# Optimization experiments

Measured on AMD Instinct MI355X. Metric: run time of the kernel, lower is better.

Reference implementation:

```python
import jax, jax.numpy as jnp
import numpy as np
import math

B, N = 1, 512
C_S, C_Z, C_H, H, PQ, PV = 384, 128, 16, 12, 4, 8
INF, EPS = 100000.0, 1e-8


def setup_inputs() -> dict:
    key = jax.random.key(0)
    ks = jax.random.split(key, 16)
    sc = 0.02
    return {
        "s": jax.random.normal(ks[0], (B, N, C_S), jnp.float32),
        "z": jax.random.normal(ks[1], (B, N, N, C_Z), jnp.float32),
        "t_trans": jax.random.normal(ks[2], (B, N, 3), jnp.float32),
        "t_rots": jax.random.normal(ks[3], (B, N, 3, 3), jnp.float32),
        "mask": jnp.ones((B, N), jnp.float32),
        "Wq": jax.random.normal(ks[4], (C_S, H * C_H), jnp.float32) * sc,
        "bq": jnp.zeros((H * C_H,), jnp.float32),
        "Wkv": jax.random.normal(ks[5], (C_S, 2 * H * C_H), jnp.float32) * sc,
        "bkv": jnp.zeros((2 * H * C_H,), jnp.float32),
        "Wqp": jax.random.normal(ks[6], (C_S, H * PQ * 3), jnp.float32) * sc,
        "bqp": jnp.zeros((H * PQ * 3,), jnp.float32),
        "Wkvp": jax.random.normal(ks[7], (C_S, H * (PQ + PV) * 3), jnp.float32) * sc,
        "bkvp": jnp.zeros((H * (PQ + PV) * 3,), jnp.float32),
        "Wb": jax.random.normal(ks[8], (C_Z, H), jnp.float32) * sc,
        "bb": jnp.zeros((H,), jnp.float32),
        "head_weights": jnp.full((H,), 0.5413, jnp.float32),  # softplus^-1(1) init
        "Wout": jax.random.normal(ks[9], (H * (C_Z + C_H + PV * 4), C_S), jnp.float32) * sc,
        "bout": jnp.zeros((C_S,), jnp.float32),
    }


def _split3_stack(x):
    # torch.split into 3 chunks along -1, then stack on new last axis -> [..., P, 3]
    return jnp.stack(jnp.split(x, 3, axis=-1), axis=-1)


def reference(s, z, t_trans, t_rots, mask, Wq, bq, Wkv, bkv, Wqp, bqp, Wkvp, bkvp,
              Wb, bb, head_weights, Wout, bout):
    q = (s @ Wq + bq).reshape(B, N, H, C_H)
    kv = (s @ Wkv + bkv).reshape(B, N, H, 2 * C_H)
    k, v = kv[..., :C_H], kv[..., C_H:]

    # point projections, moved to global frame: r @ p + t
    qp = _split3_stack(s @ Wqp + bqp)                      # [B,N,H*PQ,3] local
    qp = jnp.einsum('bnij,bnpj->bnpi', t_rots, qp) + t_trans[:, :, None, :]
    q_pts = qp.reshape(B, N, H, PQ, 3)
    kvp = _split3_stack(s @ Wkvp + bkvp)                   # [B,N,H*(PQ+PV),3]
    kvp = jnp.einsum('bnij,bnpj->bnpi', t_rots, kvp) + t_trans[:, :, None, :]
    kvp = kvp.reshape(B, N, H, PQ + PV, 3)
    k_pts, v_pts = kvp[..., :PQ, :], kvp[..., PQ:, :]

    b = z @ Wb + bb                                        # [B,N,N,H]

    a = jnp.einsum('bihc,bjhc->bhij', q, k) * math.sqrt(1.0 / (3 * C_H))
    a = a + math.sqrt(1.0 / 3) * jnp.transpose(b, (0, 3, 1, 2))

    # point-distance attention: [B,N,N,H,PQ]
    d2 = jnp.sum((q_pts[:, :, None] - k_pts[:, None]) ** 2, axis=-1)
    hw = jax.nn.softplus(head_weights) * math.sqrt(1.0 / (3 * (PQ * 9.0 / 2)))
    a = a + (-0.5) * jnp.einsum('bijhp,h->bhij', d2, hw)

    square_mask = INF * (mask[:, :, None] * mask[:, None, :] - 1.0)  # [B,N,N]
    a = jax.nn.softmax(a + square_mask[:, None], axis=-1)  # [B,H,N,N]

    o = jnp.einsum('bhij,bjhc->bihc', a, v).reshape(B, N, H * C_H)

    o_pt = jnp.einsum('bhij,bjhpx->bihpx', a, v_pts)       # [B,N,H,PV,3] global
    # invert frame: r^T @ (p - t)
    o_pt = jnp.einsum('bnji,bnhpj->bnhpi', t_rots, o_pt - t_trans[:, :, None, None, :])
    o_pt_norm = jnp.sqrt(jnp.sum(o_pt ** 2, axis=-1) + EPS).reshape(B, N, H * PV)
    o_pt = o_pt.reshape(B, N, H * PV, 3)

    o_pair = jnp.einsum('bhij,bijc->bihc', a, z).reshape(B, N, H * C_Z)

    cat = jnp.concatenate(
        [o, o_pt[..., 0], o_pt[..., 1], o_pt[..., 2], o_pt_norm, o_pair], axis=-1)
    return cat @ Wout + bout
```

## Files before the change

### kernel.cpp

```cpp
#include <hip/hip_runtime.h>
#include <math.h>

#define N 512
#define CS 384
#define CZ 128
#define CH 16
#define NH 12
#define PQ 4
#define PV 8

#define OFF_Q     0
#define OFF_K     98304
#define OFF_V     196608
#define OFF_QRAW  294912
#define OFF_KVRAW 368640
#define OFF_QPTS  589824
#define OFF_KPTS  663552
#define OFF_VPTS  737280
#define OFF_A     884736
#define OFF_CAT   4030464

__global__ __launch_bounds__(128) void proj_kernel(
    const float* __restrict__ s,
    const float* __restrict__ Wq,  const float* __restrict__ bq,
    const float* __restrict__ Wkv, const float* __restrict__ bkv,
    const float* __restrict__ Wqp, const float* __restrict__ bqp,
    const float* __restrict__ Wkvp,const float* __restrict__ bkvp,
    float* __restrict__ ws)
{
    __shared__ float st[16 * CS];
    const int n0 = blockIdx.x * 16;
    for (int idx = threadIdx.x * 4; idx < 16 * CS; idx += 128 * 4)
        *(float4*)&st[idx] = *(const float4*)&s[n0 * CS + idx];
    __syncthreads();

    const int tc = threadIdx.x & 31;
    const int tr = threadIdx.x >> 5;
    const int u0 = blockIdx.y * 128 + tc * 4;
    const int r0 = tr * 4;

    const float* W; const float* bptr; int ncol, lc0;
    if (u0 < 192)      { W = Wq;   bptr = bq;   ncol = 192; lc0 = u0; }
    else if (u0 < 576) { W = Wkv;  bptr = bkv;  ncol = 384; lc0 = u0 - 192; }
    else if (u0 < 720) { W = Wqp;  bptr = bqp;  ncol = 144; lc0 = u0 - 576; }
    else               { W = Wkvp; bptr = bkvp; ncol = 432; lc0 = u0 - 720; }

    float acc[4][4];
    #pragma unroll
    for (int r = 0; r < 4; r++)
        #pragma unroll
        for (int c = 0; c < 4; c++) acc[r][c] = 0.f;

    for (int k = 0; k < CS; k += 4) {
        float4 w0 = *(const float4*)&W[(k + 0) * ncol + lc0];
        float4 w1 = *(const float4*)&W[(k + 1) * ncol + lc0];
        float4 w2 = *(const float4*)&W[(k + 2) * ncol + lc0];
        float4 w3 = *(const float4*)&W[(k + 3) * ncol + lc0];
        #pragma unroll
        for (int r = 0; r < 4; r++) {
            float4 sv = *(const float4*)&st[(r0 + r) * CS + k];
            acc[r][0] += sv.x * w0.x + sv.y * w1.x + sv.z * w2.x + sv.w * w3.x;
            acc[r][1] += sv.x * w0.y + sv.y * w1.y + sv.z * w2.y + sv.w * w3.y;
            acc[r][2] += sv.x * w0.z + sv.y * w1.z + sv.z * w2.z + sv.w * w3.z;
            acc[r][3] += sv.x * w0.w + sv.y * w1.w + sv.z * w2.w + sv.w * w3.w;
        }
    }

    #pragma unroll
    for (int c = 0; c < 4; c++) {
        const int u = u0 + c;
        const float bias = bptr[lc0 + c];
        #pragma unroll
        for (int r = 0; r < 4; r++) {
            const int n = n0 + r0 + r;
            int oidx;
            if (u < 192) oidx = OFF_Q + n * 192 + u;
            else if (u < 576) {
                int lc = u - 192, h = lc >> 5, w = lc & 31;
                oidx = (w < 16) ? OFF_K + n * 192 + h * 16 + w
                                : OFF_V + n * 192 + h * 16 + (w - 16);
            } else if (u < 720) oidx = OFF_QRAW + n * 144 + (u - 576);
            else                oidx = OFF_KVRAW + n * 432 + (u - 720);
            ws[oidx] = acc[r][c] + bias;
        }
    }
}

__global__ __launch_bounds__(192) void point_kernel(
    const float* __restrict__ t_trans, const float* __restrict__ t_rots,
    float* __restrict__ ws)
{
    const int n = blockIdx.x;
    const int t = threadIdx.x;
    __shared__ float R[9], tr[3];
    if (t < 9) R[t] = t_rots[n * 9 + t];
    if (t < 3) tr[t] = t_trans[n * 3 + t];
    __syncthreads();

    float x0, x1, x2;
    int base;
    if (t < 48) {
        int idx = t;
        x0 = ws[OFF_QRAW + n * 144 + 0 * 48 + idx];
        x1 = ws[OFF_QRAW + n * 144 + 1 * 48 + idx];
        x2 = ws[OFF_QRAW + n * 144 + 2 * 48 + idx];
        int h = idx >> 2, p = idx & 3;
        base = OFF_QPTS + ((n * NH + h) * PQ + p) * 3;
    } else {
        int idx = t - 48;
        x0 = ws[OFF_KVRAW + n * 432 + 0 * 144 + idx];
        x1 = ws[OFF_KVRAW + n * 432 + 1 * 144 + idx];
        x2 = ws[OFF_KVRAW + n * 432 + 2 * 144 + idx];
        int h = idx / 12, p = idx % 12;
        if (p < PQ) base = OFF_KPTS + ((n * NH + h) * PQ + p) * 3;
        else        base = OFF_VPTS + ((n * NH + h) * PV + (p - PQ)) * 3;
    }
    ws[base + 0] = R[0] * x0 + R[1] * x1 + R[2] * x2 + tr[0];
    ws[base + 1] = R[3] * x0 + R[4] * x1 + R[5] * x2 + tr[1];
    ws[base + 2] = R[6] * x0 + R[7] * x1 + R[8] * x2 + tr[2];
}

__global__ __launch_bounds__(192) void logitA_kernel(
    const float* __restrict__ mask, const float* __restrict__ hweights,
    float* __restrict__ ws)
{
    const int j0 = blockIdx.x * 16;
    const int i0 = blockIdx.y * 16;
    const int t = threadIdx.x;

    __shared__ float qt[16 * 200];
    __shared__ float kt[16 * 200];
    __shared__ float qpt[16 * 148];
    __shared__ float kpt[16 * 148];
    __shared__ float mi[16], mj[16];

    {
        const float* src = ws + OFF_Q + i0 * 192;
        for (int idx = t * 4; idx < 3072; idx += 768) {
            float4 v = *(const float4*)&src[idx];
            *(float4*)&qt[(idx / 192) * 200 + idx % 192] = v;
        }
    }
    {
        const float* src = ws + OFF_K + j0 * 192;
        for (int idx = t * 4; idx < 3072; idx += 768) {
            float4 v = *(const float4*)&src[idx];
            *(float4*)&kt[(idx / 192) * 200 + idx % 192] = v;
        }
    }
    {
        const float* src = ws + OFF_QPTS + i0 * 144;
        for (int idx = t * 4; idx < 2304; idx += 768) {
            float4 v = *(const float4*)&src[idx];
            *(float4*)&qpt[(idx / 144) * 148 + idx % 144] = v;
        }
    }
    {
        const float* src = ws + OFF_KPTS + j0 * 144;
        for (int idx = t * 4; idx < 2304; idx += 768) {
            float4 v = *(const float4*)&src[idx];
            *(float4*)&kpt[(idx / 144) * 148 + idx % 144] = v;
        }
    }
    if (t < 16) { mi[t] = mask[i0 + t]; mj[t] = mask[j0 + t]; }
    __syncthreads();

    const int jj = t & 15;
    const int h = t >> 4;
    const float hw = log1pf(expf(hweights[h])) * 0.13608276348795434f;
    const float cqk = 0.14433756729740643f;

    float4 kr0 = *(const float4*)&kt[jj * 200 + h * 16 + 0];
    float4 kr1 = *(const float4*)&kt[jj * 200 + h * 16 + 4];
    float4 kr2 = *(const float4*)&kt[jj * 200 + h * 16 + 8];
    float4 kr3 = *(const float4*)&kt[jj * 200 + h * 16 + 12];
    float4 kp0 = *(const float4*)&kpt[jj * 148 + h * 12 + 0];
    float4 kp1 = *(const float4*)&kpt[jj * 148 + h * 12 + 4];
    float4 kp2 = *(const float4*)&kpt[jj * 148 + h * 12 + 8];
    const float mjv = mj[jj];

    for (int ii = 0; ii < 16; ii++) {
        float4 q0 = *(const float4*)&qt[ii * 200 + h * 16 + 0];
        float4 q1 = *(const float4*)&qt[ii * 200 + h * 16 + 4];
        float4 q2 = *(const float4*)&qt[ii * 200 + h * 16 + 8];
        float4 q3 = *(const float4*)&qt[ii * 200 + h * 16 + 12];
        float qk = q0.x * kr0.x + q0.y * kr0.y + q0.z * kr0.z + q0.w * kr0.w
                 + q1.x * kr1.x + q1.y * kr1.y + q1.z * kr1.z + q1.w * kr1.w
                 + q2.x * kr2.x + q2.y * kr2.y + q2.z * kr2.z + q2.w * kr2.w
                 + q3.x * kr3.x + q3.y * kr3.y + q3.z * kr3.z + q3.w * kr3.w;
        float4 p0 = *(const float4*)&qpt[ii * 148 + h * 12 + 0];
        float4 p1 = *(const float4*)&qpt[ii * 148 + h * 12 + 4];
        float4 p2 = *(const float4*)&qpt[ii * 148 + h * 12 + 8];
        float e, d2 = 0.f;
        e = p0.x - kp0.x; d2 += e * e;  e = p0.y - kp0.y; d2 += e * e;
        e = p0.z - kp0.z; d2 += e * e;  e = p0.w - kp0.w; d2 += e * e;
        e = p1.x - kp1.x; d2 += e * e;  e = p1.y - kp1.y; d2 += e * e;
        e = p1.z - kp1.z; d2 += e * e;  e = p1.w - kp1.w; d2 += e * e;
        e = p2.x - kp2.x; d2 += e * e;  e = p2.y - kp2.y; d2 += e * e;
        e = p2.z - kp2.z; d2 += e * e;  e = p2.w - kp2.w; d2 += e * e;
        float sm = 100000.0f * (mi[ii] * mjv - 1.0f);
        ws[OFF_A + ((size_t)(i0 + ii) * NH + h) * N + j0 + jj] =
            qk * cqk - 0.5f * hw * d2 + sm;
    }
}

__global__ __launch_bounds__(512) void bsoft_kernel(
    const float* __restrict__ z, const float* __restrict__ Wb,
    const float* __restrict__ bb, float* __restrict__ ws)
{
    const int i = blockIdx.x;
    const int t = threadIdx.x;
    __shared__ float zt[128 * 132];
    __shared__ float wbt[12 * 132];
    __shared__ float wred[8][4];

    for (int idx = t; idx < CZ * NH; idx += 512) {
        int c = idx / NH, h = idx % NH;
        wbt[h * 132 + c] = Wb[idx];
    }

    const int jj = t & 127;
    const int hg = t >> 7;
    const int h0 = hg * 3;
    const float bb0 = bb[h0], bb1 = bb[h0 + 1], bb2 = bb[h0 + 2];
    const float cb = 0.5773502691896258f;

    float lg[3][4];

    for (int T = 0; T < 4; T++) {
        __syncthreads();
        const float* zsrc = z + ((size_t)i * N + T * 128) * CZ;
        for (int idx = t * 4; idx < 16384; idx += 2048) {
            float4 v = *(const float4*)&zsrc[idx];
            *(float4*)&zt[(idx >> 7) * 132 + (idx & 127)] = v;
        }
        __syncthreads();

        float a0 = bb0, a1 = bb1, a2 = bb2;
        const float* zr = &zt[jj * 132];
        const float* w0 = &wbt[(h0 + 0) * 132];
        const float* w1 = &wbt[(h0 + 1) * 132];
        const float* w2 = &wbt[(h0 + 2) * 132];
        #pragma unroll
        for (int c = 0; c < CZ; c += 4) {
            float4 zq = *(const float4*)&zr[c];
            float4 q0 = *(const float4*)&w0[c];
            float4 q1 = *(const float4*)&w1[c];
            float4 q2 = *(const float4*)&w2[c];
            a0 += zq.x * q0.x + zq.y * q0.y + zq.z * q0.z + zq.w * q0.w;
            a1 += zq.x * q1.x + zq.y * q1.y + zq.z * q1.z + zq.w * q1.w;
            a2 += zq.x * q2.x + zq.y * q2.y + zq.z * q2.z + zq.w * q2.w;
        }
        const float* arow = ws + OFF_A + (size_t)i * NH * N + T * 128 + jj;
        lg[0][T] = arow[(size_t)(h0 + 0) * N] + cb * a0;
        lg[1][T] = arow[(size_t)(h0 + 1) * N] + cb * a1;
        lg[2][T] = arow[(size_t)(h0 + 2) * N] + cb * a2;
    }

    const int wv = t >> 6;
    float mx[3], sm[3];
    #pragma unroll
    for (int r = 0; r < 3; r++) {
        float m = fmaxf(fmaxf(lg[r][0], lg[r][1]), fmaxf(lg[r][2], lg[r][3]));
        #pragma unroll
        for (int o = 32; o > 0; o >>= 1) m = fmaxf(m, __shfl_xor(m, o));
        mx[r] = m;
    }
    if ((t & 63) == 0) {
        wred[wv][0] = mx[0]; wred[wv][1] = mx[1]; wred[wv][2] = mx[2];
    }
    __syncthreads();
    #pragma unroll
    for (int r = 0; r < 3; r++)
        mx[r] = fmaxf(wred[hg * 2][r], wred[hg * 2 + 1][r]);
    __syncthreads();
    #pragma unroll
    for (int r = 0; r < 3; r++) {
        float s = 0.f;
        #pragma unroll
        for (int T = 0; T < 4; T++) { lg[r][T] = __expf(lg[r][T] - mx[r]); s += lg[r][T]; }
        #pragma unroll
        for (int o = 32; o > 0; o >>= 1) s += __shfl_xor(s, o);
        sm[r] = s;
    }
    if ((t & 63) == 0) {
        wred[wv][0] = sm[0]; wred[wv][1] = sm[1]; wred[wv][2] = sm[2];
    }
    __syncthreads();
    #pragma unroll
    for (int r = 0; r < 3; r++) {
        float inv = 1.0f / (wred[hg * 2][r] + wred[hg * 2 + 1][r]);
        float* prow = ws + OFF_A + ((size_t)i * NH + h0 + r) * N + jj;
        #pragma unroll
        for (int T = 0; T < 4; T++)
            prow[T * 128] = lg[r][T] * inv;
    }
}

__global__ __launch_bounds__(832) void finish_kernel(
    const float* __restrict__ z, const float* __restrict__ t_trans,
    const float* __restrict__ t_rots, const float* __restrict__ ws_c,
    float* __restrict__ ws)
{
    const int i = blockIdx.x;
    const int t = threadIdx.x;
    __shared__ float a_s[12 * 520];

    {
        const float* src = ws_c + OFF_A + (size_t)i * (NH * N);
        for (int idx = t * 4; idx < NH * N; idx += 832 * 4) {
            float4 v = *(const float4*)&src[idx];
            int h = idx >> 9, j = idx & 511;
            *(float4*)&a_s[h * 520 + j] = v;
        }
    }
    __syncthreads();

    float* cat = ws + OFF_CAT + (size_t)i * 2112;

    if (t < 512) {
        const int c = t & 127, hg = t >> 7;
        const float* zrow = z + (size_t)i * N * CZ + c;
        const float* a0 = a_s + (hg + 0) * 520;
        const float* a1 = a_s + (hg + 4) * 520;
        const float* a2 = a_s + (hg + 8) * 520;
        float acc0 = 0.f, acc1 = 0.f, acc2 = 0.f;
        #pragma unroll 8
        for (int j = 0; j < N; j++) {
            float zv = zrow[(size_t)j * CZ];
            acc0 += a0[j] * zv; acc1 += a1[j] * zv; acc2 += a2[j] * zv;
        }
        cat[576 + (hg + 0) * CZ + c] = acc0;
        cat[576 + (hg + 4) * CZ + c] = acc1;
        cat[576 + (hg + 8) * CZ + c] = acc2;
    } else if (t < 704) {
        const int u = t - 512, h = u >> 4, cc = u & 15;
        const float* vcol = ws_c + OFF_V + h * 16 + cc;
        const float* ah = a_s + h * 520;
        float acc = 0.f;
        #pragma unroll 8
        for (int j = 0; j < N; j++)
            acc += ah[j] * vcol[j * 192];
        cat[h * 16 + cc] = acc;
    } else if (t < 800) {
        const int u = t - 704, h = u >> 3, p = u & 7;
        const float* vp = ws_c + OFF_VPTS + (h * PV + p) * 3;
        const float* ah = a_s + h * 520;
        float g0 = 0.f, g1 = 0.f, g2 = 0.f;
        #pragma unroll 4
        for (int j = 0; j < N; j++) {
            float av = ah[j];
            const float* vpj = vp + j * (NH * PV * 3);
            g0 += av * vpj[0]; g1 += av * vpj[1]; g2 += av * vpj[2];
        }
        float R[9], ti[3];
        #pragma unroll
        for (int x = 0; x < 9; x++) R[x] = t_rots[i * 9 + x];
        #pragma unroll
        for (int x = 0; x < 3; x++) ti[x] = t_trans[i * 3 + x];
        g0 -= ti[0]; g1 -= ti[1]; g2 -= ti[2];
        float l0 = R[0] * g0 + R[3] * g1 + R[6] * g2;
        float l1 = R[1] * g0 + R[4] * g1 + R[7] * g2;
        float l2 = R[2] * g0 + R[5] * g1 + R[8] * g2;
        float nrm = sqrtf(l0 * l0 + l1 * l1 + l2 * l2 + 1e-8f);
        int e = h * PV + p;
        cat[192 + e] = l0;
        cat[288 + e] = l1;
        cat[384 + e] = l2;
        cat[480 + e] = nrm;
    }
}

__global__ __launch_bounds__(384) void init_out_kernel(
    const float* __restrict__ bout, float* __restrict__ out)
{
    out[(size_t)blockIdx.x * 384 + threadIdx.x] = bout[threadIdx.x];
}

__global__ __launch_bounds__(384) void out_kernel(
    const float* __restrict__ Wout, const float* __restrict__ ws,
    float* __restrict__ out)
{
    const int rt = blockIdx.x;
    const int kc = blockIdx.y;
    const int t = threadIdx.x;
    __shared__ float ct[16 * 264];
    for (int idx = t * 4; idx < 16 * 264; idx += 384 * 4) {
        int rr = idx / 264, kk = idx % 264;
        *(float4*)&ct[idx] =
            *(const float4*)&ws[OFF_CAT + (size_t)(rt * 16 + rr) * 2112 + kc * 264 + kk];
    }
    __syncthreads();
    const int cq = t % 96, rg = t / 96;
    const int c0 = cq * 4;
    float acc[4][4] = {};
    const float* Wp = Wout + (size_t)kc * 264 * 384 + c0;
    for (int kk = 0; kk < 264; kk++) {
        float4 w = *(const float4*)&Wp[(size_t)kk * 384];
        #pragma unroll
        for (int r = 0; r < 4; r++) {
            float sv = ct[(rg * 4 + r) * 264 + kk];
            acc[r][0] += sv * w.x; acc[r][1] += sv * w.y;
            acc[r][2] += sv * w.z; acc[r][3] += sv * w.w;
        }
    }
    #pragma unroll
    for (int r = 0; r < 4; r++) {
        float* op = out + (size_t)(rt * 16 + rg * 4 + r) * 384 + c0;
        atomicAdd(&op[0], acc[r][0]);
        atomicAdd(&op[1], acc[r][1]);
        atomicAdd(&op[2], acc[r][2]);
        atomicAdd(&op[3], acc[r][3]);
    }
}

extern "C" void kernel_launch(void* const* d_in, const int* in_sizes, int n_in,
                              void* d_out, int out_size, void* d_ws, size_t ws_size,
                              hipStream_t stream) {
    const float* s       = (const float*)d_in[0];
    const float* z       = (const float*)d_in[1];
    const float* t_trans = (const float*)d_in[2];
    const float* t_rots  = (const float*)d_in[3];
    const float* mask    = (const float*)d_in[4];
    const float* Wq      = (const float*)d_in[5];
    const float* bq      = (const float*)d_in[6];
    const float* Wkv     = (const float*)d_in[7];
    const float* bkv     = (const float*)d_in[8];
    const float* Wqp     = (const float*)d_in[9];
    const float* bqp     = (const float*)d_in[10];
    const float* Wkvp    = (const float*)d_in[11];
    const float* bkvp    = (const float*)d_in[12];
    const float* Wb      = (const float*)d_in[13];
    const float* bb      = (const float*)d_in[14];
    const float* hweights= (const float*)d_in[15];
    const float* Wout    = (const float*)d_in[16];
    const float* bout    = (const float*)d_in[17];
    float* ws  = (float*)d_ws;
    float* out = (float*)d_out;

    init_out_kernel<<<512, 384, 0, stream>>>(bout, out);
    proj_kernel<<<dim3(32, 9), 128, 0, stream>>>(s, Wq, bq, Wkv, bkv, Wqp, bqp, Wkvp, bkvp, ws);
    point_kernel<<<512, 192, 0, stream>>>(t_trans, t_rots, ws);
    logitA_kernel<<<dim3(32, 32), 192, 0, stream>>>(mask, hweights, ws);
    bsoft_kernel<<<512, 512, 0, stream>>>(z, Wb, bb, ws);
    finish_kernel<<<512, 832, 0, stream>>>(z, t_trans, t_rots, ws, ws);
    out_kernel<<<dim3(32, 8), 384, 0, stream>>>(Wout, ws, out);
}
```

Measured before the change: 425.4 us.

## Transpose V and point layouts, restructure pair-attention reduction, split proj/out work finer

```diff
diff --git a/kernel.cpp b/kernel.cpp
--- a/kernel.cpp
+++ b/kernel.cpp
@@ -11,16 +11,32 @@
 
 #define OFF_Q     0
 #define OFF_K     98304
-#define OFF_V     196608
 #define OFF_QRAW  294912
 #define OFF_KVRAW 368640
 #define OFF_QPTS  589824
 #define OFF_KPTS  663552
-#define OFF_VPTS  737280
+#define OFF_VPX   737280
+#define OFF_VPY   786432
+#define OFF_VPZ   835584
 #define OFF_A     884736
 #define OFF_CAT   4030464
-
-__global__ __launch_bounds__(128) void proj_kernel(
+#define OFF_VT    5111808
+#define OFF_WBT   5210112
+
+__global__ __launch_bounds__(384) void init_out_kernel(
+    const float* __restrict__ bout, const float* __restrict__ Wb,
+    float* __restrict__ out, float* __restrict__ ws)
+{
+    out[(size_t)blockIdx.x * 384 + threadIdx.x] = bout[threadIdx.x];
+    if (blockIdx.x == 0) {
+        for (int idx = threadIdx.x; idx < NH * CZ; idx += 384) {
+            int h = idx >> 7, c = idx & 127;
+            ws[OFF_WBT + idx] = Wb[c * NH + h];
+        }
+    }
+}
+
+__global__ __launch_bounds__(256) void proj_kernel(
     const float* __restrict__ s,
     const float* __restrict__ Wq,  const float* __restrict__ bq,
     const float* __restrict__ Wkv, const float* __restrict__ bkv,
@@ -30,14 +46,14 @@
 {
     __shared__ float st[16 * CS];
     const int n0 = blockIdx.x * 16;
-    for (int idx = threadIdx.x * 4; idx < 16 * CS; idx += 128 * 4)
+    for (int idx = threadIdx.x * 4; idx < 16 * CS; idx += 1024)
         *(float4*)&st[idx] = *(const float4*)&s[n0 * CS + idx];
     __syncthreads();
 
     const int tc = threadIdx.x & 31;
     const int tr = threadIdx.x >> 5;
     const int u0 = blockIdx.y * 128 + tc * 4;
-    const int r0 = tr * 4;
+    const int r0 = tr * 2;
 
     const float* W; const float* bptr; int ncol, lc0;
     if (u0 < 192)      { W = Wq;   bptr = bq;   ncol = 192; lc0 = u0; }
@@ -45,9 +61,9 @@
     else if (u0 < 720) { W = Wqp;  bptr = bqp;  ncol = 144; lc0 = u0 - 576; }
     else               { W = Wkvp; bptr = bkvp; ncol = 432; lc0 = u0 - 720; }
 
-    float acc[4][4];
-    #pragma unroll
-    for (int r = 0; r < 4; r++)
+    float acc[2][4];
+    #pragma unroll
+    for (int r = 0; r < 2; r++)
         #pragma unroll
         for (int c = 0; c < 4; c++) acc[r][c] = 0.f;
 
@@ -57,7 +73,7 @@
         float4 w2 = *(const float4*)&W[(k + 2) * ncol + lc0];
         float4 w3 = *(const float4*)&W[(k + 3) * ncol + lc0];
         #pragma unroll
-        for (int r = 0; r < 4; r++) {
+        for (int r = 0; r < 2; r++) {
             float4 sv = *(const float4*)&st[(r0 + r) * CS + k];
             acc[r][0] += sv.x * w0.x + sv.y * w1.x + sv.z * w2.x + sv.w * w3.x;
             acc[r][1] += sv.x * w0.y + sv.y * w1.y + sv.z * w2.y + sv.w * w3.y;
@@ -71,14 +87,14 @@
         const int u = u0 + c;
         const float bias = bptr[lc0 + c];
         #pragma unroll
-        for (int r = 0; r < 4; r++) {
+        for (int r = 0; r < 2; r++) {
             const int n = n0 + r0 + r;
             int oidx;
             if (u < 192) oidx = OFF_Q + n * 192 + u;
             else if (u < 576) {
                 int lc = u - 192, h = lc >> 5, w = lc & 31;
                 oidx = (w < 16) ? OFF_K + n * 192 + h * 16 + w
-                                : OFF_V + n * 192 + h * 16 + (w - 16);
+                                : OFF_VT + (h * 16 + (w - 16)) * 512 + n;
             } else if (u < 720) oidx = OFF_QRAW + n * 144 + (u - 576);
             else                oidx = OFF_KVRAW + n * 432 + (u - 720);
             ws[oidx] = acc[r][c] + bias;
@@ -98,26 +114,35 @@
     __syncthreads();
 
     float x0, x1, x2;
-    int base;
     if (t < 48) {
         int idx = t;
         x0 = ws[OFF_QRAW + n * 144 + 0 * 48 + idx];
         x1 = ws[OFF_QRAW + n * 144 + 1 * 48 + idx];
         x2 = ws[OFF_QRAW + n * 144 + 2 * 48 + idx];
         int h = idx >> 2, p = idx & 3;
-        base = OFF_QPTS + ((n * NH + h) * PQ + p) * 3;
-    } else {
+        int base = OFF_QPTS + ((n * NH + h) * PQ + p) * 3;
+        ws[base + 0] = R[0] * x0 + R[1] * x1 + R[2] * x2 + tr[0];
+        ws[base + 1] = R[3] * x0 + R[4] * x1 + R[5] * x2 + tr[1];
+        ws[base + 2] = R[6] * x0 + R[7] * x1 + R[8] * x2 + tr[2];
+    } else if (t < 192) {
         int idx = t - 48;
         x0 = ws[OFF_KVRAW + n * 432 + 0 * 144 + idx];
         x1 = ws[OFF_KVRAW + n * 432 + 1 * 144 + idx];
         x2 = ws[OFF_KVRAW + n * 432 + 2 * 144 + idx];
         int h = idx / 12, p = idx % 12;
-        if (p < PQ) base = OFF_KPTS + ((n * NH + h) * PQ + p) * 3;
-        else        base = OFF_VPTS + ((n * NH + h) * PV + (p - PQ)) * 3;
-    }
-    ws[base + 0] = R[0] * x0 + R[1] * x1 + R[2] * x2 + tr[0];
-    ws[base + 1] = R[3] * x0 + R[4] * x1 + R[5] * x2 + tr[1];
-    ws[base + 2] = R[6] * x0 + R[7] * x1 + R[8] * x2 + tr[2];
+        float rx = R[0] * x0 + R[1] * x1 + R[2] * x2 + tr[0];
+        float ry = R[3] * x0 + R[4] * x1 + R[5] * x2 + tr[1];
+        float rz = R[6] * x0 + R[7] * x1 + R[8] * x2 + tr[2];
+        if (p < PQ) {
+            int base = OFF_KPTS + ((n * NH + h) * PQ + p) * 3;
+            ws[base + 0] = rx; ws[base + 1] = ry; ws[base + 2] = rz;
+        } else {
+            int e = h * PV + (p - PQ);
+            ws[OFF_VPX + e * 512 + n] = rx;
+            ws[OFF_VPY + e * 512 + n] = ry;
+            ws[OFF_VPZ + e * 512 + n] = rz;
+        }
+    }
 }
 
 __global__ __launch_bounds__(192) void logitA_kernel(
@@ -136,31 +161,23 @@
 
     {
         const float* src = ws + OFF_Q + i0 * 192;
-        for (int idx = t * 4; idx < 3072; idx += 768) {
-            float4 v = *(const float4*)&src[idx];
-            *(float4*)&qt[(idx / 192) * 200 + idx % 192] = v;
-        }
+        for (int idx = t * 4; idx < 3072; idx += 768)
+            *(float4*)&qt[(idx / 192) * 200 + idx % 192] = *(const float4*)&src[idx];
     }
     {
         const float* src = ws + OFF_K + j0 * 192;
-        for (int idx = t * 4; idx < 3072; idx += 768) {
-            float4 v = *(const float4*)&src[idx];
-            *(float4*)&kt[(idx / 192) * 200 + idx % 192] = v;
-        }
+        for (int idx = t * 4; idx < 3072; idx += 768)
+            *(float4*)&kt[(idx / 192) * 200 + idx % 192] = *(const float4*)&src[idx];
     }
     {
         const float* src = ws + OFF_QPTS + i0 * 144;
-        for (int idx = t * 4; idx < 2304; idx += 768) {
-            float4 v = *(const float4*)&src[idx];
-            *(float4*)&qpt[(idx / 144) * 148 + idx % 144] = v;
-        }
+        for (int idx = t * 4; idx < 2304; idx += 768)
+            *(float4*)&qpt[(idx / 144) * 148 + idx % 144] = *(const float4*)&src[idx];
     }
     {
         const float* src = ws + OFF_KPTS + j0 * 144;
-        for (int idx = t * 4; idx < 2304; idx += 768) {
-            float4 v = *(const float4*)&src[idx];
-            *(float4*)&kpt[(idx / 144) * 148 + idx % 144] = v;
-        }
+        for (int idx = t * 4; idx < 2304; idx += 768)
+            *(float4*)&kpt[(idx / 144) * 148 + idx % 144] = *(const float4*)&src[idx];
     }
     if (t < 16) { mi[t] = mask[i0 + t]; mj[t] = mask[j0 + t]; }
     __syncthreads();
@@ -205,42 +222,34 @@
 }
 
 __global__ __launch_bounds__(512) void bsoft_kernel(
-    const float* __restrict__ z, const float* __restrict__ Wb,
-    const float* __restrict__ bb, float* __restrict__ ws)
+    const float* __restrict__ z, const float* __restrict__ bb,
+    float* ws)
 {
     const int i = blockIdx.x;
     const int t = threadIdx.x;
     __shared__ float zt[128 * 132];
-    __shared__ float wbt[12 * 132];
     __shared__ float wred[8][4];
 
-    for (int idx = t; idx < CZ * NH; idx += 512) {
-        int c = idx / NH, h = idx % NH;
-        wbt[h * 132 + c] = Wb[idx];
-    }
-
     const int jj = t & 127;
-    const int hg = t >> 7;
+    const int hg = __builtin_amdgcn_readfirstlane(t >> 7);
     const int h0 = hg * 3;
     const float bb0 = bb[h0], bb1 = bb[h0 + 1], bb2 = bb[h0 + 2];
     const float cb = 0.5773502691896258f;
+    const float* w0 = ws + OFF_WBT + (h0 + 0) * 128;
+    const float* w1 = ws + OFF_WBT + (h0 + 1) * 128;
+    const float* w2 = ws + OFF_WBT + (h0 + 2) * 128;
 
     float lg[3][4];
 
     for (int T = 0; T < 4; T++) {
         __syncthreads();
         const float* zsrc = z + ((size_t)i * N + T * 128) * CZ;
-        for (int idx = t * 4; idx < 16384; idx += 2048) {
-            float4 v = *(const float4*)&zsrc[idx];
-            *(float4*)&zt[(idx >> 7) * 132 + (idx & 127)] = v;
-        }
+        for (int idx = t * 4; idx < 16384; idx += 2048)
+            *(float4*)&zt[(idx >> 7) * 132 + (idx & 127)] = *(const float4*)&zsrc[idx];
         __syncthreads();
 
         float a0 = bb0, a1 = bb1, a2 = bb2;
         const float* zr = &zt[jj * 132];
-        const float* w0 = &wbt[(h0 + 0) * 132];
-        const float* w1 = &wbt[(h0 + 1) * 132];
-        const float* w2 = &wbt[(h0 + 2) * 132];
         #pragma unroll
         for (int c = 0; c < CZ; c += 4) {
             float4 zq = *(const float4*)&zr[c];
@@ -266,9 +275,7 @@
         for (int o = 32; o > 0; o >>= 1) m = fmaxf(m, __shfl_xor(m, o));
         mx[r] = m;
     }
-    if ((t & 63) == 0) {
-        wred[wv][0] = mx[0]; wred[wv][1] = mx[1]; wred[wv][2] = mx[2];
-    }
+    if ((t & 63) == 0) { wred[wv][0] = mx[0]; wred[wv][1] = mx[1]; wred[wv][2] = mx[2]; }
     __syncthreads();
     #pragma unroll
     for (int r = 0; r < 3; r++)
@@ -283,9 +290,7 @@
         for (int o = 32; o > 0; o >>= 1) s += __shfl_xor(s, o);
         sm[r] = s;
     }
-    if ((t & 63) == 0) {
-        wred[wv][0] = sm[0]; wred[wv][1] = sm[1]; wred[wv][2] = sm[2];
-    }
+    if ((t & 63) == 0) { wred[wv][0] = sm[0]; wred[wv][1] = sm[1]; wred[wv][2] = sm[2]; }
     __syncthreads();
     #pragma unroll
     for (int r = 0; r < 3; r++) {
@@ -299,59 +304,63 @@
 
 __global__ __launch_bounds__(832) void finish_kernel(
     const float* __restrict__ z, const float* __restrict__ t_trans,
-    const float* __restrict__ t_rots, const float* __restrict__ ws_c,
-    float* __restrict__ ws)
+    const float* __restrict__ t_rots, const float* ws_c,
+    float* ws)
 {
     const int i = blockIdx.x;
     const int t = threadIdx.x;
-    __shared__ float a_s[12 * 520];
-
-    {
-        const float* src = ws_c + OFF_A + (size_t)i * (NH * N);
-        for (int idx = t * 4; idx < NH * N; idx += 832 * 4) {
-            float4 v = *(const float4*)&src[idx];
-            int h = idx >> 9, j = idx & 511;
-            *(float4*)&a_s[h * 520 + j] = v;
-        }
-    }
-    __syncthreads();
+    __shared__ float red[128 * 48];
 
     float* cat = ws + OFF_CAT + (size_t)i * 2112;
+    const float* probs = ws_c + OFF_A + (size_t)i * NH * N;
 
     if (t < 512) {
-        const int c = t & 127, hg = t >> 7;
-        const float* zrow = z + (size_t)i * N * CZ + c;
-        const float* a0 = a_s + (hg + 0) * 520;
-        const float* a1 = a_s + (hg + 4) * 520;
-        const float* a2 = a_s + (hg + 8) * 520;
-        float acc0 = 0.f, acc1 = 0.f, acc2 = 0.f;
-        #pragma unroll 8
-        for (int j = 0; j < N; j++) {
-            float zv = zrow[(size_t)j * CZ];
-            acc0 += a0[j] * zv; acc1 += a1[j] * zv; acc2 += a2[j] * zv;
-        }
-        cat[576 + (hg + 0) * CZ + c] = acc0;
-        cat[576 + (hg + 4) * CZ + c] = acc1;
-        cat[576 + (hg + 8) * CZ + c] = acc2;
+        const int c = t & 127;
+        const int jq = __builtin_amdgcn_readfirstlane(t >> 7);
+        float op[12];
+        #pragma unroll
+        for (int h = 0; h < 12; h++) op[h] = 0.f;
+        const float* zc = z + ((size_t)i * N + jq * 128) * CZ + c;
+        const float* ab = probs + jq * 128;
+        for (int j0 = 0; j0 < 128; j0 += 4) {
+            float zv0 = zc[(size_t)(j0 + 0) * CZ];
+            float zv1 = zc[(size_t)(j0 + 1) * CZ];
+            float zv2 = zc[(size_t)(j0 + 2) * CZ];
+            float zv3 = zc[(size_t)(j0 + 3) * CZ];
+            #pragma unroll
+            for (int h = 0; h < 12; h++) {
+                float4 av = *(const float4*)&ab[h * N + j0];
+                op[h] += av.x * zv0 + av.y * zv1 + av.z * zv2 + av.w * zv3;
+            }
+        }
+        #pragma unroll
+        for (int h = 0; h < 12; h++) red[c * 48 + jq * 12 + h] = op[h];
     } else if (t < 704) {
         const int u = t - 512, h = u >> 4, cc = u & 15;
-        const float* vcol = ws_c + OFF_V + h * 16 + cc;
-        const float* ah = a_s + h * 520;
+        const float* vt = ws_c + OFF_VT + (h * 16 + cc) * 512;
+        const float* ah = probs + h * N;
         float acc = 0.f;
-        #pragma unroll 8
-        for (int j = 0; j < N; j++)
-            acc += ah[j] * vcol[j * 192];
+        for (int j = 0; j < N; j += 4) {
+            float4 av = *(const float4*)&ah[j];
+            float4 vv = *(const float4*)&vt[j];
+            acc += av.x * vv.x + av.y * vv.y + av.z * vv.z + av.w * vv.w;
+        }
         cat[h * 16 + cc] = acc;
     } else if (t < 800) {
-        const int u = t - 704, h = u >> 3, p = u & 7;
-        const float* vp = ws_c + OFF_VPTS + (h * PV + p) * 3;
-        const float* ah = a_s + h * 520;
+        const int u = t - 704, h = u >> 3;
+        const float* vx = ws_c + OFF_VPX + u * 512;
+        const float* vy = ws_c + OFF_VPY + u * 512;
+        const float* vz = ws_c + OFF_VPZ + u * 512;
+        const float* ah = probs + h * N;
         float g0 = 0.f, g1 = 0.f, g2 = 0.f;
-        #pragma unroll 4
-        for (int j = 0; j < N; j++) {
-            float av = ah[j];
-            const float* vpj = vp + j * (NH * PV * 3);
-            g0 += av * vpj[0]; g1 += av * vpj[1]; g2 += av * vpj[2];
+        for (int j = 0; j < N; j += 4) {
+            float4 av = *(const float4*)&ah[j];
+            float4 x4 = *(const float4*)&vx[j];
+            float4 y4 = *(const float4*)&vy[j];
+            float4 z4 = *(const float4*)&vz[j];
+            g0 += av.x * x4.x + av.y * x4.y + av.z * x4.z + av.w * x4.w;
+            g1 += av.x * y4.x + av.y * y4.y + av.z * y4.z + av.w * y4.w;
+            g2 += av.x * z4.x + av.y * z4.y + av.z * z4.z + av.w * z4.w;
         }
         float R[9], ti[3];
         #pragma unroll
@@ -363,18 +372,22 @@
         float l1 = R[1] * g0 + R[4] * g1 + R[7] * g2;
         float l2 = R[2] * g0 + R[5] * g1 + R[8] * g2;
         float nrm = sqrtf(l0 * l0 + l1 * l1 + l2 * l2 + 1e-8f);
-        int e = h * PV + p;
-        cat[192 + e] = l0;
-        cat[288 + e] = l1;
-        cat[384 + e] = l2;
-        cat[480 + e] = nrm;
-    }
-}
-
-__global__ __launch_bounds__(384) void init_out_kernel(
-    const float* __restrict__ bout, float* __restrict__ out)
-{
-    out[(size_t)blockIdx.x * 384 + threadIdx.x] = bout[threadIdx.x];
+        cat[192 + u] = l0;
+        cat[288 + u] = l1;
+        cat[384 + u] = l2;
+        cat[480 + u] = nrm;
+    }
+    __syncthreads();
+    if (t < 512) {
+        const int c = t & 127, hg2 = t >> 7;
+        #pragma unroll
+        for (int r = 0; r < 3; r++) {
+            int h = hg2 * 3 + r;
+            float v = red[c * 48 + 0 * 12 + h] + red[c * 48 + 1 * 12 + h]
+                    + red[c * 48 + 2 * 12 + h] + red[c * 48 + 3 * 12 + h];
+            cat[576 + h * CZ + c] = v;
+        }
+    }
 }
 
 __global__ __launch_bounds__(384) void out_kernel(
@@ -384,29 +397,27 @@
     const int rt = blockIdx.x;
     const int kc = blockIdx.y;
     const int t = threadIdx.x;
-    __shared__ float ct[16 * 264];
-    for (int idx = t * 4; idx < 16 * 264; idx += 384 * 4) {
+    __shared__ float ct[8 * 264];
+    for (int idx = t * 4; idx < 8 * 264; idx += 1536) {
         int rr = idx / 264, kk = idx % 264;
         *(float4*)&ct[idx] =
-            *(const float4*)&ws[OFF_CAT + (size_t)(rt * 16 + rr) * 2112 + kc * 264 + kk];
+            *(const float4*)&ws[OFF_CAT + (size_t)(rt * 8 + rr) * 2112 + kc * 264 + kk];
     }
     __syncthreads();
     const int cq = t % 96, rg = t / 96;
     const int c0 = cq * 4;
-    float acc[4][4] = {};
+    float acc[2][4] = {};
     const float* Wp = Wout + (size_t)kc * 264 * 384 + c0;
     for (int kk = 0; kk < 264; kk++) {
         float4 w = *(const float4*)&Wp[(size_t)kk * 384];
-        #pragma unroll
-        for (int r = 0; r < 4; r++) {
-            float sv = ct[(rg * 4 + r) * 264 + kk];
-            acc[r][0] += sv * w.x; acc[r][1] += sv * w.y;
-            acc[r][2] += sv * w.z; acc[r][3] += sv * w.w;
-        }
-    }
-    #pragma unroll
-    for (int r = 0; r < 4; r++) {
-        float* op = out + (size_t)(rt * 16 + rg * 4 + r) * 384 + c0;
+        float s0 = ct[(rg * 2 + 0) * 264 + kk];
+        float s1 = ct[(rg * 2 + 1) * 264 + kk];
+        acc[0][0] += s0 * w.x; acc[0][1] += s0 * w.y; acc[0][2] += s0 * w.z; acc[0][3] += s0 * w.w;
+        acc[1][0] += s1 * w.x; acc[1][1] += s1 * w.y; acc[1][2] += s1 * w.z; acc[1][3] += s1 * w.w;
+    }
+    #pragma unroll
+    for (int r = 0; r < 2; r++) {
+        float* op = out + (size_t)(rt * 8 + rg * 2 + r) * 384 + c0;
         atomicAdd(&op[0], acc[r][0]);
         atomicAdd(&op[1], acc[r][1]);
         atomicAdd(&op[2], acc[r][2]);
@@ -438,11 +449,11 @@
     float* ws  = (float*)d_ws;
     float* out = (float*)d_out;
 
-    init_out_kernel<<<512, 384, 0, stream>>>(bout, out);
-    proj_kernel<<<dim3(32, 9), 128, 0, stream>>>(s, Wq, bq, Wkv, bkv, Wqp, bqp, Wkvp, bkvp, ws);
+    init_out_kernel<<<512, 384, 0, stream>>>(bout, Wb, out, ws);
+    proj_kernel<<<dim3(32, 9), 256, 0, stream>>>(s, Wq, bq, Wkv, bkv, Wqp, bqp, Wkvp, bkvp, ws);
     point_kernel<<<512, 192, 0, stream>>>(t_trans, t_rots, ws);
     logitA_kernel<<<dim3(32, 32), 192, 0, stream>>>(mask, hweights, ws);
-    bsoft_kernel<<<512, 512, 0, stream>>>(z, Wb, bb, ws);
+    bsoft_kernel<<<512, 512, 0, stream>>>(z, bb, ws);
     finish_kernel<<<512, 832, 0, stream>>>(z, t_trans, t_rots, ws, ws);
-    out_kernel<<<dim3(32, 8), 384, 0, stream>>>(Wout, ws, out);
-}
+    out_kernel<<<dim3(64, 8), 384, 0, stream>>>(Wout, ws, out);
+}
```

Measured after the change: 487.7 us. +14.6%, slower.
